# Kernel tuning notes

Measured on AMD Instinct MI355X. Metric: run time of the kernel, lower is better.

## Reference

```python
import jax, jax.numpy as jnp
import numpy as np

B, L, S, D, H = 4, 1024, 1024, 1024, 16
HD = D // H  # head_dim = 64


def setup_inputs() -> dict:
    key = jax.random.key(0)
    ks = jax.random.split(key, 12)
    s = 1.0 / np.sqrt(D)
    return {
        "query": jax.random.normal(ks[0], (B, L, D), jnp.float32),
        "key": jax.random.normal(ks[1], (B, S, D), jnp.float32),
        "value": jax.random.normal(ks[2], (B, S, D), jnp.float32),
        "key_padding_mask": jax.random.randint(ks[3], (B, S), 0, 2) > 0,
        "Wq": jax.random.normal(ks[4], (D, D), jnp.float32) * s,
        "bq": jnp.zeros((D,), jnp.float32),
        "Wk": jax.random.normal(ks[5], (D, D), jnp.float32) * s,
        "bk": jnp.zeros((D,), jnp.float32),
        "Wv": jax.random.normal(ks[6], (D, D), jnp.float32) * s,
        "bv": jnp.zeros((D,), jnp.float32),
        "Wo": jax.random.normal(ks[7], (D, D), jnp.float32) * s,
        "bo": jnp.zeros((D,), jnp.float32),
    }


def reference(query, key, value, key_padding_mask, Wq, bq, Wk, bk, Wv, bv, Wo, bo):
    bs, tgt, _ = query.shape
    src = key.shape[1]
    # Q/K/V projections (nn.Linear: x @ W.T + b)
    q = query @ Wq.T + bq
    k = key @ Wk.T + bk
    v = value @ Wv.T + bv
    # split heads: (B, T, H, HD)
    q = q.reshape(bs, tgt, H, HD)
    k = k.reshape(bs, src, H, HD)
    v = v.reshape(bs, src, H, HD)
    # scaled dot-product attention with key padding mask (True = masked)
    scale = 1.0 / jnp.sqrt(jnp.asarray(HD, q.dtype))
    scores = jnp.einsum("blhd,bshd->bhls", q, k) * scale  # (B,H,L,S)
    neg_inf = jnp.asarray(-jnp.inf, scores.dtype)
    scores = scores + jnp.where(key_padding_mask[:, None, None, :], neg_inf, 0.0)
    attn = jax.nn.softmax(scores, axis=-1)
    out = jnp.einsum("bhls,bshd->blhd", attn, v).reshape(bs, tgt, D)
    return out @ Wo.T + bo
```

## Files before the change

### kernel.cpp

```cpp
#include <hip/hip_runtime.h>
#include <hip/hip_bf16.h>


typedef __bf16 bf16;
typedef __bf16 bf16x8 __attribute__((ext_vector_type(8)));
typedef float floatx4 __attribute__((ext_vector_type(4)));

#define D_MODEL 1024
#define NHEAD   16
#define HDIM    64
#define BATCH   4
#define SEQ     1024
#define M_ROWS  (BATCH * SEQ)
#define ACT_N   ((size_t)M_ROWS * D_MODEL)
#define W_N     ((size_t)D_MODEL * D_MODEL)
#define SC2     0.18033688011112042f

#define GLD(gp, lp) __builtin_amdgcn_global_load_lds( \
    (__attribute__((address_space(1))) void*)(gp), \
    (__attribute__((address_space(3))) void*)(lp), 16, 0, 0)

__global__ __launch_bounds__(256)
void k_convert_all(const float* __restrict__ a0, const float* __restrict__ a1,
                   const float* __restrict__ a2,
                   const float* __restrict__ w0, const float* __restrict__ w1,
                   const float* __restrict__ w2, const float* __restrict__ w3,
                   bf16* __restrict__ dst,
                   const unsigned* __restrict__ m, float* __restrict__ mbias)
{
    if (blockIdx.x == 8192) {
        __shared__ unsigned viol[4];
        __shared__ int fmsh;
        if (threadIdx.x < 4) viol[threadIdx.x] = 0;
        __syncthreads();
        unsigned a = 0, b = 0, c = 0, d = 0;
        for (int i = threadIdx.x; i < 1024; i += 256) {
            unsigned v = m[i];
            if (v > 1u) a = 1;
            if (((v & 0xFFu) > 1u) || (((v >> 8) & 0xFFu) > 1u) ||
                (((v >> 16) & 0xFFu) > 1u) || (((v >> 24) & 0xFFu) > 1u)) b = 1;
            unsigned lo = v & 0xFFFFu, hi = v >> 16;
            if (!((lo == 0u || lo == 0x3F80u) && (hi == 0u || hi == 0x3F80u))) c = 1;
            if (lo != 0u) d = 1;
        }
        if (a) atomicOr(&viol[0], 1u);
        if (b) atomicOr(&viol[1], 1u);
        if (c) atomicOr(&viol[2], 1u);
        if (d) atomicOr(&viol[3], 1u);
        __syncthreads();
        if (threadIdx.x == 0) {
            int fm;
            if (!viol[0])      fm = 1;
            else if (!viol[1]) fm = 0;
            else if (!viol[2]) fm = viol[3] ? 2 : 3;
            else               fm = 0;
            fmsh = fm;
        }
        __syncthreads();
        const int fm = fmsh;
        for (int i = 0; i < 16; ++i) {
            int s = i * 256 + threadIdx.x;
            bool msk;
            if (fm == 1)      msk = ((const int*)m)[s] != 0;
            else if (fm == 2) msk = ((const unsigned short*)m)[s] != 0;
            else if (fm == 3) msk = ((const unsigned*)m)[s] != 0;
            else              msk = ((const unsigned char*)m)[s] != 0;
            mbias[s] = msk ? -1e30f : 0.f;
        }
        return;
    }

    size_t i = ((size_t)blockIdx.x * 256 + threadIdx.x) * 8;
    const float* src; size_t off;
    if (i < ((size_t)12 << 20)) {
        int z = (int)(i >> 22);
        src = (z == 0) ? a0 : (z == 1) ? a1 : a2;
        off = i & (((size_t)1 << 22) - 1);
    } else {
        size_t r = i - ((size_t)12 << 20);
        int j = (int)(r >> 20);
        src = (j == 0) ? w0 : (j == 1) ? w1 : (j == 2) ? w2 : w3;
        off = r & (((size_t)1 << 20) - 1);
    }
    float4 f0 = ((const float4*)(src + off))[0];
    float4 f1 = ((const float4*)(src + off))[1];
    bf16x8 o;
    o[0] = (bf16)f0.x; o[1] = (bf16)f0.y; o[2] = (bf16)f0.z; o[3] = (bf16)f0.w;
    o[4] = (bf16)f1.x; o[5] = (bf16)f1.y; o[6] = (bf16)f1.z; o[7] = (bf16)f1.w;
    *(bf16x8*)(dst + i) = o;
}

template<typename CT>
__device__ __forceinline__ void gemm_core(const bf16* __restrict__ A,
                                          const bf16* __restrict__ W,
                                          const float* __restrict__ bias,
                                          CT* __restrict__ C,
                                          int m0, int n0, bool rowBias)
{
    __shared__ alignas(16) bf16 As[128 * 32];
    __shared__ alignas(16) bf16 Bs[128 * 32];

    const int t    = threadIdx.x;
    const int lane = t & 63;
    const int w    = t >> 6;
    const int wm   = w >> 1, wn = w & 1;
    const int l15  = lane & 15;
    const int quad = lane >> 4;

    floatx4 acc[4][4] = {};

    for (int k0 = 0; k0 < D_MODEL; k0 += 32) {
        #pragma unroll
        for (int i = 0; i < 2; ++i) {
            int c   = i * 256 + t;
            int row = c >> 2, cb = (c & 3) * 8;
            const bf16* ga = A + (size_t)(m0 + row) * D_MODEL + k0 + cb;
            const bf16* gb = W + (size_t)(n0 + row) * D_MODEL + k0 + cb;
            int lo = (i * 256 + w * 64) * 8;
            GLD(ga, As + lo);
            GLD(gb, Bs + lo);
        }
        __syncthreads();

        bf16x8 af[4], bfr[4];
        #pragma unroll
        for (int i = 0; i < 4; ++i)
            af[i] = *(const bf16x8*)&As[(wm * 64 + i * 16 + l15) * 32 + quad * 8];
        #pragma unroll
        for (int j = 0; j < 4; ++j)
            bfr[j] = *(const bf16x8*)&Bs[(wn * 64 + j * 16 + l15) * 32 + quad * 8];

        #pragma unroll
        for (int i = 0; i < 4; ++i)
            #pragma unroll
            for (int j = 0; j < 4; ++j)
                acc[i][j] = __builtin_amdgcn_mfma_f32_16x16x32_bf16(
                    af[i], bfr[j], acc[i][j], 0, 0, 0);
        __syncthreads();
    }

    #pragma unroll
    for (int i = 0; i < 4; ++i) {
        int rowb = m0 + wm * 64 + i * 16 + quad * 4;
        float bvr[4];
        if (rowBias) {
            #pragma unroll
            for (int r = 0; r < 4; ++r) bvr[r] = bias[rowb + r];
        }
        #pragma unroll
        for (int j = 0; j < 4; ++j) {
            int col = n0 + wn * 64 + j * 16 + l15;
            float bc = rowBias ? 0.f : bias[col];
            #pragma unroll
            for (int r = 0; r < 4; ++r) {
                float val = acc[i][j][r] + (rowBias ? bvr[r] : bc);
                C[(size_t)(rowb + r) * D_MODEL + col] = (CT)val;
            }
        }
    }
}

__global__ __launch_bounds__(256)
void k_gemm_proj(const bf16* __restrict__ cq, const bf16* __restrict__ ck,
                 const bf16* __restrict__ cv,
                 const bf16* __restrict__ cWq, const bf16* __restrict__ cWk,
                 const bf16* __restrict__ cWv,
                 const float* __restrict__ bq, const float* __restrict__ bk,
                 const float* __restrict__ bv,
                 bf16* __restrict__ qproj, bf16* __restrict__ kproj,
                 bf16* __restrict__ vt)
{
    const int bid = blockIdx.x;
    const int x = bid & 7;
    const int j = bid >> 3;
    const int p = x * 12 + (j >> 3);
    const int n0 = (j & 7) * 128;
    if (p < 64) {
        int z = p >> 5, m0 = (p & 31) * 128;
        gemm_core<bf16>(z ? ck : cq, z ? cWk : cWq, z ? bk : bq,
                        z ? kproj : qproj, m0, n0, false);
    } else {
        int pv = p - 64;
        int b = pv >> 3, m0 = (pv & 7) * 128;
        gemm_core<bf16>(cWv, cv + (size_t)b * W_N, bv,
                        vt + (size_t)b * W_N, m0, n0, true);
    }
}

__global__ __launch_bounds__(256)
void k_gemm_o(const bf16* __restrict__ A, const bf16* __restrict__ W,
              const float* __restrict__ bb, float* __restrict__ C)
{
    const int bid = blockIdx.x;
    const int x = bid & 7;
    const int j = bid >> 3;
    const int p = x * 4 + (j >> 3);
    const int n0 = (j & 7) * 128;
    gemm_core<float>(A, W, bb, C, p * 128, n0, false);
}

__global__ __launch_bounds__(256)
void k_attn(const bf16* __restrict__ qproj, const bf16* __restrict__ kproj,
            const bf16* __restrict__ vt, const float* __restrict__ mbias_g,
            bf16* __restrict__ ctx)
{
    __shared__ alignas(16) bf16 Qst[4096];
    __shared__ alignas(16) bf16 Kst[4096];
    __shared__ alignas(16) bf16 Vst[4096];
    __shared__ alignas(16) bf16 Past[4096];
    __shared__ float MB[1024];

    const int t    = threadIdx.x;
    const int lane = t & 63;
    const int w    = t >> 6;
    const int l15  = lane & 15;
    const int quad = lane >> 4;

    const int b  = blockIdx.x >> 4;
    const int h  = blockIdx.x & 15;
    const int q0 = blockIdx.y * 64;

    #pragma unroll
    for (int i = 0; i < 4; ++i)
        MB[i * 256 + t] = mbias_g[b * SEQ + i * 256 + t];

    #pragma unroll
    for (int kk = 0; kk < 2; ++kk) {
        const bf16* gp = qproj + (size_t)(b * SEQ + q0 + w * 16 + l15) * D_MODEL
                       + h * HDIM + kk * 32 + quad * 8;
        GLD(gp, Qst + (w * 2 + kk) * 512);
    }
    __syncthreads();

    bf16x8 qf[2];
    #pragma unroll
    for (int kk = 0; kk < 2; ++kk)
        qf[kk] = *(const bf16x8*)&Qst[(w * 2 + kk) * 512 + lane * 8];

    bf16x8 ones;
    #pragma unroll
    for (int e = 0; e < 8; ++e) ones[e] = (bf16)1.0f;

    floatx4 o[4] = {};
    floatx4 accl = {};

    const int pbase = w * 1024 + (l15 >> 3) * 128 + quad * 32 + (l15 & 7);

    for (int s0 = 0; s0 < SEQ; s0 += 64) {
        __syncthreads();
        #pragma unroll
        for (int i = 0; i < 2; ++i) {
            int f = w * 2 + i;
            int row = (f >> 1) * 16 + l15;
            int cb  = (f & 1) * 32 + quad * 8;
            GLD(kproj + (size_t)(b * SEQ + s0 + row) * D_MODEL + h * HDIM + cb,
                Kst + f * 512);
            GLD(vt + (size_t)(b * 1024 + h * HDIM + row) * D_MODEL + s0 + cb,
                Vst + f * 512);
        }
        __syncthreads();

        floatx4 s_acc[4] = {};
        #pragma unroll
        for (int j = 0; j < 4; ++j)
            #pragma unroll
            for (int kk = 0; kk < 2; ++kk) {
                bf16x8 kf = *(const bf16x8*)&Kst[(j * 2 + kk) * 512 + lane * 8];
                s_acc[j] = __builtin_amdgcn_mfma_f32_16x16x32_bf16(
                    qf[kk], kf, s_acc[j], 0, 0, 0);
            }

        #pragma unroll
        for (int j = 0; j < 4; ++j) {
            float mb = MB[s0 + j * 16 + l15];
            #pragma unroll
            for (int r = 0; r < 4; ++r) {
                float p = __builtin_amdgcn_exp2f(fmaf(s_acc[j][r], SC2, mb));
                Past[pbase + (j >> 1) * 512 + (j & 1) * 256 + r * 8] = (bf16)p;
            }
        }
        __builtin_amdgcn_wave_barrier();

        bf16x8 pf[2];
        #pragma unroll
        for (int kk = 0; kk < 2; ++kk)
            pf[kk] = *(const bf16x8*)&Past[w * 1024 + kk * 512 + lane * 8];

        #pragma unroll
        for (int kk = 0; kk < 2; ++kk)
            accl = __builtin_amdgcn_mfma_f32_16x16x32_bf16(pf[kk], ones, accl,
                                                           0, 0, 0);
        #pragma unroll
        for (int j = 0; j < 4; ++j)
            #pragma unroll
            for (int kk = 0; kk < 2; ++kk) {
                bf16x8 vf = *(const bf16x8*)&Vst[(j * 2 + kk) * 512 + lane * 8];
                o[j] = __builtin_amdgcn_mfma_f32_16x16x32_bf16(
                    pf[kk], vf, o[j], 0, 0, 0);
            }
    }

    float inv[4];
    #pragma unroll
    for (int r = 0; r < 4; ++r) inv[r] = (accl[r] > 0.f) ? 1.f / accl[r] : 0.f;
    #pragma unroll
    for (int j = 0; j < 4; ++j)
        #pragma unroll
        for (int r = 0; r < 4; ++r) {
            int row = q0 + w * 16 + quad * 4 + r;
            int col = h * HDIM + j * 16 + l15;
            ctx[(size_t)(b * SEQ + row) * D_MODEL + col] = (bf16)(o[j][r] * inv[r]);
        }
}

extern "C" void kernel_launch(void* const* d_in, const int* in_sizes, int n_in,
                              void* d_out, int out_size, void* d_ws, size_t ws_size,
                              hipStream_t stream)
{
    char* wsb = (char*)d_ws;
    float* mbias = (float*)wsb;
    bf16* cbase = (bf16*)(wsb + 65536);
    bf16 *cq = cbase, *ck = cq + ACT_N, *cv = ck + ACT_N;
    bf16 *cWq = cv + ACT_N, *cWk = cWq + W_N, *cWv = cWk + W_N, *cWo = cWv + W_N;
    bf16* qproj = cWo + W_N;
    bf16* kproj = qproj + ACT_N;
    bf16* vt    = kproj + ACT_N;
    bf16* ctx   = vt + ACT_N;
    float* out  = (float*)d_out;

    k_convert_all<<<8193, 256, 0, stream>>>(
        (const float*)d_in[0], (const float*)d_in[1], (const float*)d_in[2],
        (const float*)d_in[4], (const float*)d_in[6], (const float*)d_in[8],
        (const float*)d_in[10], cbase, (const unsigned*)d_in[3], mbias);

    k_gemm_proj<<<768, 256, 0, stream>>>(cq, ck, cv, cWq, cWk, cWv,
                                         (const float*)d_in[5],
                                         (const float*)d_in[7],
                                         (const float*)d_in[9],
                                         qproj, kproj, vt);
    k_attn<<<dim3(64, 16), 256, 0, stream>>>(qproj, kproj, vt, mbias, ctx);
    k_gemm_o<<<256, 256, 0, stream>>>(ctx, cWo, (const float*)d_in[11], out);
}
```

Before: 235.1 us.

## Double-buffer LDS tiles in GEMM and attention, swizzle GEMM LDS layout

```diff
diff --git a/kernel.cpp b/kernel.cpp
--- a/kernel.cpp
+++ b/kernel.cpp
@@ -97,8 +97,8 @@
                                           CT* __restrict__ C,
                                           int m0, int n0, bool rowBias)
 {
-    __shared__ alignas(16) bf16 As[128 * 32];
-    __shared__ alignas(16) bf16 Bs[128 * 32];
+    __shared__ alignas(16) bf16 As[2][128 * 32];
+    __shared__ alignas(16) bf16 Bs[2][128 * 32];
 
     const int t    = threadIdx.x;
     const int lane = t & 63;
@@ -109,26 +109,42 @@
 
     floatx4 acc[4][4] = {};
 
+    #pragma unroll
+    for (int i = 0; i < 2; ++i) {
+        int c   = i * 256 + t;
+        int row = c >> 2;
+        int ck  = ((c & 3) ^ ((row >> 1) & 3)) * 8;
+        int lo  = (i * 256 + w * 64) * 8;
+        GLD(A + (size_t)(m0 + row) * D_MODEL + ck, As[0] + lo);
+        GLD(W + (size_t)(n0 + row) * D_MODEL + ck, Bs[0] + lo);
+    }
+    __syncthreads();
+
+    int cur = 0;
     for (int k0 = 0; k0 < D_MODEL; k0 += 32) {
-        #pragma unroll
-        for (int i = 0; i < 2; ++i) {
-            int c   = i * 256 + t;
-            int row = c >> 2, cb = (c & 3) * 8;
-            const bf16* ga = A + (size_t)(m0 + row) * D_MODEL + k0 + cb;
-            const bf16* gb = W + (size_t)(n0 + row) * D_MODEL + k0 + cb;
-            int lo = (i * 256 + w * 64) * 8;
-            GLD(ga, As + lo);
-            GLD(gb, Bs + lo);
-        }
-        __syncthreads();
+        if (k0 + 32 < D_MODEL) {
+            #pragma unroll
+            for (int i = 0; i < 2; ++i) {
+                int c   = i * 256 + t;
+                int row = c >> 2;
+                int ck  = ((c & 3) ^ ((row >> 1) & 3)) * 8;
+                int lo  = (i * 256 + w * 64) * 8;
+                GLD(A + (size_t)(m0 + row) * D_MODEL + k0 + 32 + ck, As[cur ^ 1] + lo);
+                GLD(W + (size_t)(n0 + row) * D_MODEL + k0 + 32 + ck, Bs[cur ^ 1] + lo);
+            }
+        }
 
         bf16x8 af[4], bfr[4];
         #pragma unroll
-        for (int i = 0; i < 4; ++i)
-            af[i] = *(const bf16x8*)&As[(wm * 64 + i * 16 + l15) * 32 + quad * 8];
-        #pragma unroll
-        for (int j = 0; j < 4; ++j)
-            bfr[j] = *(const bf16x8*)&Bs[(wn * 64 + j * 16 + l15) * 32 + quad * 8];
+        for (int i = 0; i < 4; ++i) {
+            int r = wm * 64 + i * 16 + l15;
+            af[i] = *(const bf16x8*)&As[cur][r * 32 + (quad ^ ((r >> 1) & 3)) * 8];
+        }
+        #pragma unroll
+        for (int j = 0; j < 4; ++j) {
+            int r = wn * 64 + j * 16 + l15;
+            bfr[j] = *(const bf16x8*)&Bs[cur][r * 32 + (quad ^ ((r >> 1) & 3)) * 8];
+        }
 
         #pragma unroll
         for (int i = 0; i < 4; ++i)
@@ -136,7 +152,9 @@
             for (int j = 0; j < 4; ++j)
                 acc[i][j] = __builtin_amdgcn_mfma_f32_16x16x32_bf16(
                     af[i], bfr[j], acc[i][j], 0, 0, 0);
-        __syncthreads();
+
+        __syncthreads();
+        cur ^= 1;
     }
 
     #pragma unroll
@@ -204,11 +222,9 @@
             const bf16* __restrict__ vt, const float* __restrict__ mbias_g,
             bf16* __restrict__ ctx)
 {
-    __shared__ alignas(16) bf16 Qst[4096];
-    __shared__ alignas(16) bf16 Kst[4096];
-    __shared__ alignas(16) bf16 Vst[4096];
+    __shared__ alignas(16) bf16 Kst[2][4096];
+    __shared__ alignas(16) bf16 Vst[2][4096];
     __shared__ alignas(16) bf16 Past[4096];
-    __shared__ float MB[1024];
 
     const int t    = threadIdx.x;
     const int lane = t & 63;
@@ -221,21 +237,27 @@
     const int q0 = blockIdx.y * 64;
 
     #pragma unroll
-    for (int i = 0; i < 4; ++i)
-        MB[i * 256 + t] = mbias_g[b * SEQ + i * 256 + t];
-
-    #pragma unroll
     for (int kk = 0; kk < 2; ++kk) {
         const bf16* gp = qproj + (size_t)(b * SEQ + q0 + w * 16 + l15) * D_MODEL
                        + h * HDIM + kk * 32 + quad * 8;
-        GLD(gp, Qst + (w * 2 + kk) * 512);
+        GLD(gp, Past + (w * 2 + kk) * 512);
+    }
+    #pragma unroll
+    for (int i = 0; i < 2; ++i) {
+        int f   = w * 2 + i;
+        int row = (f >> 1) * 16 + l15;
+        int cb  = (f & 1) * 32 + quad * 8;
+        GLD(kproj + (size_t)(b * SEQ + row) * D_MODEL + h * HDIM + cb,
+            Kst[0] + f * 512);
+        GLD(vt + (size_t)(b * 1024 + h * HDIM + row) * D_MODEL + cb,
+            Vst[0] + f * 512);
     }
     __syncthreads();
 
     bf16x8 qf[2];
     #pragma unroll
     for (int kk = 0; kk < 2; ++kk)
-        qf[kk] = *(const bf16x8*)&Qst[(w * 2 + kk) * 512 + lane * 8];
+        qf[kk] = *(const bf16x8*)&Past[(w * 2 + kk) * 512 + lane * 8];
 
     bf16x8 ones;
     #pragma unroll
@@ -245,34 +267,38 @@
     floatx4 accl = {};
 
     const int pbase = w * 1024 + (l15 >> 3) * 128 + quad * 32 + (l15 & 7);
-
+    const float* __restrict__ mbb = mbias_g + b * SEQ;
+
+    int cur = 0;
     for (int s0 = 0; s0 < SEQ; s0 += 64) {
-        __syncthreads();
-        #pragma unroll
-        for (int i = 0; i < 2; ++i) {
-            int f = w * 2 + i;
-            int row = (f >> 1) * 16 + l15;
-            int cb  = (f & 1) * 32 + quad * 8;
-            GLD(kproj + (size_t)(b * SEQ + s0 + row) * D_MODEL + h * HDIM + cb,
-                Kst + f * 512);
-            GLD(vt + (size_t)(b * 1024 + h * HDIM + row) * D_MODEL + s0 + cb,
-                Vst + f * 512);
-        }
-        __syncthreads();
+        if (s0 + 64 < SEQ) {
+            #pragma unroll
+            for (int i = 0; i < 2; ++i) {
+                int f   = w * 2 + i;
+                int row = (f >> 1) * 16 + l15;
+                int cb  = (f & 1) * 32 + quad * 8;
+                GLD(kproj + (size_t)(b * SEQ + s0 + 64 + row) * D_MODEL
+                        + h * HDIM + cb,
+                    Kst[cur ^ 1] + f * 512);
+                GLD(vt + (size_t)(b * 1024 + h * HDIM + row) * D_MODEL
+                        + s0 + 64 + cb,
+                    Vst[cur ^ 1] + f * 512);
+            }
+        }
 
         floatx4 s_acc[4] = {};
         #pragma unroll
         for (int j = 0; j < 4; ++j)
             #pragma unroll
             for (int kk = 0; kk < 2; ++kk) {
-                bf16x8 kf = *(const bf16x8*)&Kst[(j * 2 + kk) * 512 + lane * 8];
+                bf16x8 kf = *(const bf16x8*)&Kst[cur][(j * 2 + kk) * 512 + lane * 8];
                 s_acc[j] = __builtin_amdgcn_mfma_f32_16x16x32_bf16(
                     qf[kk], kf, s_acc[j], 0, 0, 0);
             }
 
         #pragma unroll
         for (int j = 0; j < 4; ++j) {
-            float mb = MB[s0 + j * 16 + l15];
+            float mb = mbb[s0 + j * 16 + l15];
             #pragma unroll
             for (int r = 0; r < 4; ++r) {
                 float p = __builtin_amdgcn_exp2f(fmaf(s_acc[j][r], SC2, mb));
@@ -294,10 +320,13 @@
         for (int j = 0; j < 4; ++j)
             #pragma unroll
             for (int kk = 0; kk < 2; ++kk) {
-                bf16x8 vf = *(const bf16x8*)&Vst[(j * 2 + kk) * 512 + lane * 8];
+                bf16x8 vf = *(const bf16x8*)&Vst[cur][(j * 2 + kk) * 512 + lane * 8];
                 o[j] = __builtin_amdgcn_mfma_f32_16x16x32_bf16(
                     pf[kk], vf, o[j], 0, 0, 0);
             }
+
+        __syncthreads();
+        cur ^= 1;
     }
 
     float inv[4];
```

New measurement: 236.5 us. About the same (+0.6%).
